# Performance work log

Hardware: AMD Instinct MI355X
Metric: run time of the kernel (lower is better)

Reference implementation:

```python
import jax, jax.numpy as jnp
import numpy as np

N, F_IN, F_OUT, K = 16384, 64, 64, 3


def setup_inputs() -> dict:
    key = jax.random.key(0)
    k1, k2, k3, k4 = jax.random.split(key, 4)
    x = jax.random.normal(k1, (N, F_IN), dtype=jnp.float32)
    # dense rescaled Laplacian; scale so repeated matmuls stay numerically tame
    L_tilde = jax.random.normal(k2, (N, N), dtype=jnp.float32) / np.float32(np.sqrt(N))
    stdv = 1.0 / np.sqrt(F_OUT)
    weights = jax.random.uniform(k3, (K + 1, F_IN, F_OUT), dtype=jnp.float32,
                                 minval=-stdv, maxval=stdv)
    bias = jax.random.uniform(k4, (F_OUT,), dtype=jnp.float32, minval=-stdv, maxval=stdv)
    return {"x": x, "L_tilde": L_tilde, "weights": weights, "bias": bias}


def reference(x, L_tilde, weights, bias):
    # Chebyshev recurrence: T0 = x, T1 = L@x, Tk = 2*L@T_{k-1} - T_{k-2}
    T_prev = x                                   # (N, F_in)
    out = T_prev @ weights[0]                    # (N, F_out)
    T_curr = L_tilde @ x
    out = out + T_curr @ weights[1]
    for k in range(2, K + 1):                    # fixed small K: python loop is fine
        T_next = 2.0 * (L_tilde @ T_curr) - T_prev
        out = out + T_next @ weights[k]
        T_prev, T_curr = T_curr, T_next
    return out + bias
```

## Files before the change

kernel.cpp:

```cpp
#include <hip/hip_runtime.h>
#include <cstddef>
#include <cstdint>

#define NN 16384
#define FF 64
#define BM 64
#define BK 64
#define SK 2
#define KHALF (NN / SK)
#define NC (KHALF / BK)

typedef __attribute__((ext_vector_type(8))) short bf16x8;
typedef __attribute__((ext_vector_type(4))) float f32x4;
typedef unsigned short ushort_t;

#define GLOBAL_AS __attribute__((address_space(1)))
#define LDS_AS    __attribute__((address_space(3)))

__device__ __forceinline__ void f32_split(float f, ushort_t& h, ushort_t& l) {
    unsigned u = __builtin_bit_cast(unsigned, f);
    h = (ushort_t)(u >> 16);
    float hf = __builtin_bit_cast(float, u & 0xFFFF0000u);
    float lo = f - hf;
    l = (ushort_t)(__builtin_bit_cast(unsigned, lo) >> 16);
}

__global__ __launch_bounds__(256) void convT(const float* __restrict__ T,
                                             ushort_t* __restrict__ Th,
                                             ushort_t* __restrict__ Tl)
{
    __shared__ float S[64][68];
    const int t = threadIdx.x;
    const int rb = blockIdx.x * 64;
    {
        const int row = t >> 2;
        const int c0 = (t & 3) * 16;
        const float* src = T + (size_t)(rb + row) * FF + c0;
        *(float4*)&S[row][c0 + 0]  = *(const float4*)(src + 0);
        *(float4*)&S[row][c0 + 4]  = *(const float4*)(src + 4);
        *(float4*)&S[row][c0 + 8]  = *(const float4*)(src + 8);
        *(float4*)&S[row][c0 + 12] = *(const float4*)(src + 12);
    }
    __syncthreads();
    const int cc = t >> 2;
    const int r0 = (t & 3) * 16;
    ushort_t hh[16], ll[16];
#pragma unroll
    for (int i = 0; i < 16; ++i)
        f32_split(S[r0 + i][cc], hh[i], ll[i]);
    unsigned wh[8], wl[8];
#pragma unroll
    for (int j = 0; j < 8; ++j) {
        wh[j] = (unsigned)hh[2 * j] | ((unsigned)hh[2 * j + 1] << 16);
        wl[j] = (unsigned)ll[2 * j] | ((unsigned)ll[2 * j + 1] << 16);
    }
    const size_t o = (size_t)cc * NN + rb + r0;
    *(uint4*)(Th + o)     = make_uint4(wh[0], wh[1], wh[2], wh[3]);
    *(uint4*)(Th + o + 8) = make_uint4(wh[4], wh[5], wh[6], wh[7]);
    *(uint4*)(Tl + o)     = make_uint4(wl[0], wl[1], wl[2], wl[3]);
    *(uint4*)(Tl + o + 8) = make_uint4(wl[4], wl[5], wl[6], wl[7]);
}

__global__ __launch_bounds__(256) void cheb_gemm_mfma(
    const float* __restrict__ L, const ushort_t* __restrict__ Th,
    const ushort_t* __restrict__ Tl, float* __restrict__ P)
{
    __shared__ ushort_t Ah[2][BM * BK];
    __shared__ ushort_t Al[2][BM * BK];
    __shared__ ushort_t Bh[2][FF * BK];
    __shared__ ushort_t Bl[2][FF * BK];

    const int tid  = threadIdx.x;
    const int lane = tid & 63;
    const int w    = tid >> 6;
    const int s    = blockIdx.x >> 8;
    const int m    = blockIdx.x & 255;
    const int row0g = m * BM;
    const int kbase = s * KHALF;

    const int wm = w >> 1, wn = w & 1;
    const int frow = lane & 15;
    const int fk8  = (lane >> 4) * 8;

    const int arow = w * 4 + (lane >> 4);
    const int akq  = lane & 15;
    const int axor = (arow & 7) << 4;

    const ushort_t* Tsrc = (w & 1) ? Tl : Th;
    const int boct0 = (w >> 1) * 4;

    f32x4 acc[2][2];
#pragma unroll
    for (int i = 0; i < 2; ++i)
#pragma unroll
        for (int j = 0; j < 2; ++j) acc[i][j] = (f32x4)0.f;

    float4 va[4];

    const float* Labase = L + (size_t)(row0g + arow) * NN + kbase + akq * 4;

#define ISSUE_B(c, slot)                                                        \
    {                                                                           \
        const size_t kc = (size_t)(c) * BK;                                     \
        char* bbase = (char*)((w & 1) ? Bl[slot] : Bh[slot]);                   \
        _Pragma("unroll")                                                       \
        for (int o = 0; o < 4; ++o) {                                           \
            const int oct = boct0 + o;                                          \
            const int col = oct * 8 + (lane >> 3);                              \
            const ushort_t* g = Tsrc + (size_t)col * NN + kbase + kc            \
                                + (((lane & 7) ^ (col & 7)) * 8);               \
            __builtin_amdgcn_global_load_lds((const GLOBAL_AS void*)g,          \
                (LDS_AS void*)(bbase + oct * 1024), 16, 0, 0);                  \
        }                                                                       \
    }

#define LOAD_A(c)                                                               \
    {                                                                           \
        const float* g = Labase + (size_t)(c) * BK;                             \
        va[0] = *(const float4*)(g);                                            \
        va[1] = *(const float4*)(g + (size_t)16 * NN);                          \
        va[2] = *(const float4*)(g + (size_t)32 * NN);                          \
        va[3] = *(const float4*)(g + (size_t)48 * NN);                          \
    }

#define CONV_WRITE_A(slot)                                                      \
    {                                                                           \
        char* ahb = (char*)Ah[slot];                                            \
        char* alb = (char*)Al[slot];                                            \
        _Pragma("unroll")                                                       \
        for (int p = 0; p < 4; ++p) {                                           \
            const int r = arow + p * 16;                                        \
            ushort_t h0, h1, h2, h3, l0, l1, l2, l3;                            \
            f32_split(va[p].x, h0, l0);                                         \
            f32_split(va[p].y, h1, l1);                                         \
            f32_split(va[p].z, h2, l2);                                         \
            f32_split(va[p].w, h3, l3);                                         \
            const unsigned hi01 = (unsigned)h0 | ((unsigned)h1 << 16);          \
            const unsigned hi23 = (unsigned)h2 | ((unsigned)h3 << 16);          \
            const unsigned lo01 = (unsigned)l0 | ((unsigned)l1 << 16);          \
            const unsigned lo23 = (unsigned)l2 | ((unsigned)l3 << 16);          \
            const int byte = (r * 128 + akq * 8) ^ axor;                        \
            *(uint2*)(ahb + byte) = make_uint2(hi01, hi23);                     \
            *(uint2*)(alb + byte) = make_uint2(lo01, lo23);                     \
        }                                                                       \
    }

    ISSUE_B(0, 0)
    LOAD_A(0)
    CONV_WRITE_A(0)
    __syncthreads();

    for (int c = 0; c < NC; ++c) {
        const int slot = c & 1;
        if (c + 1 < NC) {
            ISSUE_B(c + 1, slot ^ 1)
            LOAD_A(c + 1)
        }
        {
            const char* ahb = (const char*)Ah[slot];
            const char* alb = (const char*)Al[slot];
            const char* bhb = (const char*)Bh[slot];
            const char* blb = (const char*)Bl[slot];
#pragma unroll
            for (int ks = 0; ks < 2; ++ks) {
                const int kk = ks * 32 + fk8;
                bf16x8 Afh[2], Afl[2], Bfh[2], Bfl[2];
#pragma unroll
                for (int mt = 0; mt < 2; ++mt) {
                    const int row = wm * 32 + mt * 16 + frow;
                    const int off = (row * 128 + kk * 2) ^ ((row & 7) << 4);
                    Afh[mt] = *(const bf16x8*)(ahb + off);
                    Afl[mt] = *(const bf16x8*)(alb + off);
                }
#pragma unroll
                for (int nt = 0; nt < 2; ++nt) {
                    const int col = wn * 32 + nt * 16 + frow;
                    const int off = (col * 128 + kk * 2) ^ ((col & 7) << 4);
                    Bfh[nt] = *(const bf16x8*)(bhb + off);
                    Bfl[nt] = *(const bf16x8*)(blb + off);
                }
#pragma unroll
                for (int mt = 0; mt < 2; ++mt)
#pragma unroll
                    for (int nt = 0; nt < 2; ++nt) {
                        acc[mt][nt] = __builtin_amdgcn_mfma_f32_16x16x32_bf16(
                            Afh[mt], Bfh[nt], acc[mt][nt], 0, 0, 0);
                        acc[mt][nt] = __builtin_amdgcn_mfma_f32_16x16x32_bf16(
                            Afh[mt], Bfl[nt], acc[mt][nt], 0, 0, 0);
                        acc[mt][nt] = __builtin_amdgcn_mfma_f32_16x16x32_bf16(
                            Afl[mt], Bfh[nt], acc[mt][nt], 0, 0, 0);
                    }
            }
        }
        if (c + 1 < NC) CONV_WRITE_A(slot ^ 1)
        __syncthreads();
    }

    float* Pp = P + (size_t)s * NN * FF;
#pragma unroll
    for (int mt = 0; mt < 2; ++mt)
#pragma unroll
        for (int nt = 0; nt < 2; ++nt) {
            const int row = row0g + wm * 32 + mt * 16 + (lane >> 4) * 4;
            const int col = wn * 32 + nt * 16 + frow;
#pragma unroll
            for (int r = 0; r < 4; ++r)
                Pp[(size_t)(row + r) * FF + col] = acc[mt][nt][r];
        }
#undef ISSUE_B
#undef LOAD_A
#undef CONV_WRITE_A
}

__global__ __launch_bounds__(256) void reduce_axpby(
    const float* __restrict__ P0, const float* __restrict__ P1,
    const float* __restrict__ Tsub, float* __restrict__ Tout,
    float alpha, float beta)
{
    const int total = NN * FF / 4;
    for (int i = blockIdx.x * blockDim.x + threadIdx.x; i < total;
         i += gridDim.x * blockDim.x) {
        const float4 p0 = ((const float4*)P0)[i];
        const float4 p1 = ((const float4*)P1)[i];
        const float4 ts = ((const float4*)Tsub)[i];
        float4 o;
        o.x = alpha * (p0.x + p1.x) + beta * ts.x;
        o.y = alpha * (p0.y + p1.y) + beta * ts.y;
        o.z = alpha * (p0.z + p1.z) + beta * ts.z;
        o.w = alpha * (p0.w + p1.w) + beta * ts.w;
        ((float4*)Tout)[i] = o;
    }
}

__global__ __launch_bounds__(256) void out_update(
    const float* __restrict__ T, const float* __restrict__ Wk,
    const float* __restrict__ bias, float* __restrict__ out, int init)
{
    const int row = blockIdx.x * 4 + (threadIdx.x >> 6);
    const int col = threadIdx.x & 63;
    const float* t = T + (size_t)row * FF;
    const size_t oi = (size_t)row * FF + col;

    float acc = init ? bias[col] : out[oi];
#pragma unroll
    for (int f = 0; f < FF; ++f)
        acc += t[f] * Wk[f * FF + col];
    out[oi] = acc;
}

extern "C" void kernel_launch(void* const* d_in, const int* in_sizes, int n_in,
                              void* d_out, int out_size, void* d_ws, size_t ws_size,
                              hipStream_t stream)
{
    const float* x    = (const float*)d_in[0];
    const float* L    = (const float*)d_in[1];
    const float* W    = (const float*)d_in[2];
    const float* bias = (const float*)d_in[3];
    float* out = (float*)d_out;

    const size_t M1 = (size_t)NN * FF;
    float* wsf = (float*)d_ws;
    float* T1 = wsf;
    float* T2 = wsf + M1;
    float* T3 = wsf + 2 * M1;
    float* P0 = wsf + 3 * M1;
    float* P1 = wsf + 4 * M1;
    ushort_t* Tht = (ushort_t*)(wsf + 5 * M1);
    ushort_t* Tlt = Tht + M1;

    const dim3 gg(256 * SK), bg(256);
    const dim3 gc(NN / 64),  bc(256);
    const dim3 gr(512),      br(256);
    const dim3 go(NN / 4),   bo(256);

    out_update<<<go, bo, 0, stream>>>(x, W + 0 * FF * FF, bias, out, 1);

    convT<<<gc, bc, 0, stream>>>(x, Tht, Tlt);
    cheb_gemm_mfma<<<gg, bg, 0, stream>>>(L, Tht, Tlt, P0);
    reduce_axpby<<<gr, br, 0, stream>>>(P0, P1, x, T1, 1.f, 0.f);
    out_update<<<go, bo, 0, stream>>>(T1, W + 1 * FF * FF, bias, out, 0);

    convT<<<gc, bc, 0, stream>>>(T1, Tht, Tlt);
    cheb_gemm_mfma<<<gg, bg, 0, stream>>>(L, Tht, Tlt, P0);
    reduce_axpby<<<gr, br, 0, stream>>>(P0, P1, x, T2, 2.f, -1.f);
    out_update<<<go, bo, 0, stream>>>(T2, W + 2 * FF * FF, bias, out, 0);

    convT<<<gc, bc, 0, stream>>>(T2, Tht, Tlt);
    cheb_gemm_mfma<<<gg, bg, 0, stream>>>(L, Tht, Tlt, P0);
    reduce_axpby<<<gr, br, 0, stream>>>(P0, P1, T1, T3, 2.f, -1.f);
    out_update<<<go, bo, 0, stream>>>(T3, W + 3 * FF * FF, bias, out, 0);
}
```

Measured before the change: 747.5 us.

## Fuse reduce, output GEMM and bf16 split into one post-hop kernel; split-K 4

Replaces the separate reduce_axpby, out_update and convT launches after each Laplacian GEMM with a single post_hop kernel. Per 64-row tile it sums the split-K partials, applies the Chebyshev axpby, accumulates into the output through the weight matrix staged in LDS, and writes the transposed bf16 hi/lo operands for the next hop. The x@W0 term and the bias are folded into the first hop. Split-K goes from 2 to 4, giving the GEMM more blocks at the cost of more partial-sum traffic. Intermediates T2 and T3 are no longer stored, which cuts global memory round trips and launch count.

```diff
diff --git a/kernel.cpp b/kernel.cpp
--- a/kernel.cpp
+++ b/kernel.cpp
@@ -6,9 +6,9 @@
 #define FF 64
 #define BM 64
 #define BK 64
-#define SK 2
-#define KHALF (NN / SK)
-#define NC (KHALF / BK)
+#define SK 4
+#define KQ (NN / SK)
+#define NC (KQ / BK)
 
 typedef __attribute__((ext_vector_type(8))) short bf16x8;
 typedef __attribute__((ext_vector_type(4))) float f32x4;
@@ -76,7 +76,7 @@
     const int s    = blockIdx.x >> 8;
     const int m    = blockIdx.x & 255;
     const int row0g = m * BM;
-    const int kbase = s * KHALF;
+    const int kbase = s * KQ;
 
     const int wm = w >> 1, wn = w & 1;
     const int frow = lane & 15;
@@ -212,40 +212,162 @@
 #undef CONV_WRITE_A
 }
 
-__global__ __launch_bounds__(256) void reduce_axpby(
-    const float* __restrict__ P0, const float* __restrict__ P1,
-    const float* __restrict__ Tsub, float* __restrict__ Tout,
+__global__ __launch_bounds__(256) void post_hop(
+    const float* __restrict__ P,
+    const float* __restrict__ Tsub,
+    const float* __restrict__ Xin,
+    const float* __restrict__ W0w,
+    const float* __restrict__ Wkw,
+    const float* __restrict__ bias,
+    float* __restrict__ Tout,
+    ushort_t* __restrict__ Th, ushort_t* __restrict__ Tl,
+    float* __restrict__ out,
     float alpha, float beta)
 {
-    const int total = NN * FF / 4;
-    for (int i = blockIdx.x * blockDim.x + threadIdx.x; i < total;
-         i += gridDim.x * blockDim.x) {
-        const float4 p0 = ((const float4*)P0)[i];
-        const float4 p1 = ((const float4*)P1)[i];
-        const float4 ts = ((const float4*)Tsub)[i];
-        float4 o;
-        o.x = alpha * (p0.x + p1.x) + beta * ts.x;
-        o.y = alpha * (p0.y + p1.y) + beta * ts.y;
-        o.z = alpha * (p0.z + p1.z) + beta * ts.z;
-        o.w = alpha * (p0.w + p1.w) + beta * ts.w;
-        ((float4*)Tout)[i] = o;
-    }
-}
-
-__global__ __launch_bounds__(256) void out_update(
-    const float* __restrict__ T, const float* __restrict__ Wk,
-    const float* __restrict__ bias, float* __restrict__ out, int init)
-{
-    const int row = blockIdx.x * 4 + (threadIdx.x >> 6);
-    const int col = threadIdx.x & 63;
-    const float* t = T + (size_t)row * FF;
-    const size_t oi = (size_t)row * FF + col;
-
-    float acc = init ? bias[col] : out[oi];
-#pragma unroll
-    for (int f = 0; f < FF; ++f)
-        acc += t[f] * Wk[f * FF + col];
-    out[oi] = acc;
+    __shared__ float ST[64][68];
+    __shared__ float ST2[64][68];
+    __shared__ float WK[64][64];
+    __shared__ float WX[64][64];
+
+    const int tid = threadIdx.x;
+    const int rb = blockIdx.x * 64;
+    const size_t M1 = (size_t)NN * FF;
+
+    {
+        float4* wd = (float4*)&WK[0][0];
+        const float4* ws = (const float4*)Wkw;
+#pragma unroll
+        for (int j = 0; j < 4; ++j) wd[tid * 4 + j] = ws[tid * 4 + j];
+        if (Xin) {
+            float4* xd = (float4*)&WX[0][0];
+            const float4* xs = (const float4*)W0w;
+#pragma unroll
+            for (int j = 0; j < 4; ++j) xd[tid * 4 + j] = xs[tid * 4 + j];
+        }
+    }
+
+    {
+        const int arow = tid >> 2;
+        const int ac0 = (tid & 3) * 16;
+        const size_t rowOff = (size_t)(rb + arow) * FF + ac0;
+#pragma unroll
+        for (int j = 0; j < 4; ++j) {
+            const size_t o = rowOff + 4 * j;
+            float4 s  = *(const float4*)(P + o);
+            float4 p1 = *(const float4*)(P + M1 + o);
+            float4 p2 = *(const float4*)(P + 2 * M1 + o);
+            float4 p3 = *(const float4*)(P + 3 * M1 + o);
+            s.x += p1.x + p2.x + p3.x; s.y += p1.y + p2.y + p3.y;
+            s.z += p1.z + p2.z + p3.z; s.w += p1.w + p2.w + p3.w;
+            float4 t;
+            t.x = alpha * s.x; t.y = alpha * s.y;
+            t.z = alpha * s.z; t.w = alpha * s.w;
+            if (beta != 0.f) {
+                const float4 ts = *(const float4*)(Tsub + o);
+                t.x += beta * ts.x; t.y += beta * ts.y;
+                t.z += beta * ts.z; t.w += beta * ts.w;
+            }
+            if (Tout) *(float4*)(Tout + o) = t;
+            const int f0 = ac0 + 4 * j;
+            ST[f0 + 0][arow] = t.x; ST[f0 + 1][arow] = t.y;
+            ST[f0 + 2][arow] = t.z; ST[f0 + 3][arow] = t.w;
+            if (Xin) {
+                const float4 xv = *(const float4*)(Xin + o);
+                ST2[f0 + 0][arow] = xv.x; ST2[f0 + 1][arow] = xv.y;
+                ST2[f0 + 2][arow] = xv.z; ST2[f0 + 3][arow] = xv.w;
+            }
+        }
+    }
+    __syncthreads();
+
+    if (Th) {
+        const int cc = tid >> 2;
+        const int r0 = (tid & 3) * 16;
+        float vals[16];
+        *(float4*)&vals[0]  = *(const float4*)&ST[cc][r0];
+        *(float4*)&vals[4]  = *(const float4*)&ST[cc][r0 + 4];
+        *(float4*)&vals[8]  = *(const float4*)&ST[cc][r0 + 8];
+        *(float4*)&vals[12] = *(const float4*)&ST[cc][r0 + 12];
+        ushort_t hh[16], ll[16];
+#pragma unroll
+        for (int i = 0; i < 16; ++i) f32_split(vals[i], hh[i], ll[i]);
+        unsigned wh[8], wl[8];
+#pragma unroll
+        for (int j = 0; j < 8; ++j) {
+            wh[j] = (unsigned)hh[2 * j] | ((unsigned)hh[2 * j + 1] << 16);
+            wl[j] = (unsigned)ll[2 * j] | ((unsigned)ll[2 * j + 1] << 16);
+        }
+        const size_t o = (size_t)cc * NN + rb + r0;
+        *(uint4*)(Th + o)     = make_uint4(wh[0], wh[1], wh[2], wh[3]);
+        *(uint4*)(Th + o + 8) = make_uint4(wh[4], wh[5], wh[6], wh[7]);
+        *(uint4*)(Tl + o)     = make_uint4(wl[0], wl[1], wl[2], wl[3]);
+        *(uint4*)(Tl + o + 8) = make_uint4(wl[4], wl[5], wl[6], wl[7]);
+    }
+
+    {
+        const int tx = tid & 7;
+        const int ty = tid >> 3;
+        const int col0 = tx * 8;
+        const int row0 = ty * 2;
+        float acc[2][8];
+        if (Xin) {
+            const float4 b0 = *(const float4*)(bias + col0);
+            const float4 b1 = *(const float4*)(bias + col0 + 4);
+#pragma unroll
+            for (int r = 0; r < 2; ++r) {
+                acc[r][0] = b0.x; acc[r][1] = b0.y; acc[r][2] = b0.z; acc[r][3] = b0.w;
+                acc[r][4] = b1.x; acc[r][5] = b1.y; acc[r][6] = b1.z; acc[r][7] = b1.w;
+            }
+        } else {
+#pragma unroll
+            for (int r = 0; r < 2; ++r) {
+                const size_t o = (size_t)(rb + row0 + r) * FF + col0;
+                const float4 o0 = *(const float4*)(out + o);
+                const float4 o1 = *(const float4*)(out + o + 4);
+                acc[r][0] = o0.x; acc[r][1] = o0.y; acc[r][2] = o0.z; acc[r][3] = o0.w;
+                acc[r][4] = o1.x; acc[r][5] = o1.y; acc[r][6] = o1.z; acc[r][7] = o1.w;
+            }
+        }
+#pragma unroll
+        for (int f = 0; f < FF; ++f) {
+            const float2 lv = *(const float2*)&ST[f][row0];
+            const float4 w0 = *(const float4*)&WK[f][col0];
+            const float4 w1 = *(const float4*)&WK[f][col0 + 4];
+            acc[0][0] += lv.x * w0.x; acc[0][1] += lv.x * w0.y;
+            acc[0][2] += lv.x * w0.z; acc[0][3] += lv.x * w0.w;
+            acc[0][4] += lv.x * w1.x; acc[0][5] += lv.x * w1.y;
+            acc[0][6] += lv.x * w1.z; acc[0][7] += lv.x * w1.w;
+            acc[1][0] += lv.y * w0.x; acc[1][1] += lv.y * w0.y;
+            acc[1][2] += lv.y * w0.z; acc[1][3] += lv.y * w0.w;
+            acc[1][4] += lv.y * w1.x; acc[1][5] += lv.y * w1.y;
+            acc[1][6] += lv.y * w1.z; acc[1][7] += lv.y * w1.w;
+        }
+        if (Xin) {
+#pragma unroll
+            for (int f = 0; f < FF; ++f) {
+                const float2 lv = *(const float2*)&ST2[f][row0];
+                const float4 w0 = *(const float4*)&WX[f][col0];
+                const float4 w1 = *(const float4*)&WX[f][col0 + 4];
+                acc[0][0] += lv.x * w0.x; acc[0][1] += lv.x * w0.y;
+                acc[0][2] += lv.x * w0.z; acc[0][3] += lv.x * w0.w;
+                acc[0][4] += lv.x * w1.x; acc[0][5] += lv.x * w1.y;
+                acc[0][6] += lv.x * w1.z; acc[0][7] += lv.x * w1.w;
+                acc[1][0] += lv.y * w0.x; acc[1][1] += lv.y * w0.y;
+                acc[1][2] += lv.y * w0.z; acc[1][3] += lv.y * w0.w;
+                acc[1][4] += lv.y * w1.x; acc[1][5] += lv.y * w1.y;
+                acc[1][6] += lv.y * w1.z; acc[1][7] += lv.y * w1.w;
+            }
+        }
+#pragma unroll
+        for (int r = 0; r < 2; ++r) {
+            const size_t o = (size_t)(rb + row0 + r) * FF + col0;
+            float4 v0, v1;
+            v0.x = acc[r][0]; v0.y = acc[r][1]; v0.z = acc[r][2]; v0.w = acc[r][3];
+            v1.x = acc[r][4]; v1.y = acc[r][5]; v1.z = acc[r][6]; v1.w = acc[r][7];
+            *(float4*)(out + o) = v0;
+            *(float4*)(out + o + 4) = v1;
+        }
+    }
 }
 
 extern "C" void kernel_launch(void* const* d_in, const int* in_sizes, int n_in,
@@ -261,32 +383,21 @@
     const size_t M1 = (size_t)NN * FF;
     float* wsf = (float*)d_ws;
     float* T1 = wsf;
-    float* T2 = wsf + M1;
-    float* T3 = wsf + 2 * M1;
-    float* P0 = wsf + 3 * M1;
-    float* P1 = wsf + 4 * M1;
+    float* P  = wsf + M1;
     ushort_t* Tht = (ushort_t*)(wsf + 5 * M1);
     ushort_t* Tlt = Tht + M1;
 
     const dim3 gg(256 * SK), bg(256);
     const dim3 gc(NN / 64),  bc(256);
-    const dim3 gr(512),      br(256);
-    const dim3 go(NN / 4),   bo(256);
-
-    out_update<<<go, bo, 0, stream>>>(x, W + 0 * FF * FF, bias, out, 1);
 
     convT<<<gc, bc, 0, stream>>>(x, Tht, Tlt);
-    cheb_gemm_mfma<<<gg, bg, 0, stream>>>(L, Tht, Tlt, P0);
-    reduce_axpby<<<gr, br, 0, stream>>>(P0, P1, x, T1, 1.f, 0.f);
-    out_update<<<go, bo, 0, stream>>>(T1, W + 1 * FF * FF, bias, out, 0);
-
-    convT<<<gc, bc, 0, stream>>>(T1, Tht, Tlt);
-    cheb_gemm_mfma<<<gg, bg, 0, stream>>>(L, Tht, Tlt, P0);
-    reduce_axpby<<<gr, br, 0, stream>>>(P0, P1, x, T2, 2.f, -1.f);
-    out_update<<<go, bo, 0, stream>>>(T2, W + 2 * FF * FF, bias, out, 0);
-
-    convT<<<gc, bc, 0, stream>>>(T2, Tht, Tlt);
-    cheb_gemm_mfma<<<gg, bg, 0, stream>>>(L, Tht, Tlt, P0);
-    reduce_axpby<<<gr, br, 0, stream>>>(P0, P1, T1, T3, 2.f, -1.f);
-    out_update<<<go, bo, 0, stream>>>(T3, W + 3 * FF * FF, bias, out, 0);
+    cheb_gemm_mfma<<<gg, bg, 0, stream>>>(L, Tht, Tlt, P);
+    post_hop<<<gc, bc, 0, stream>>>(P, x, x, W + 0 * FF * FF, W + 1 * FF * FF,
+                                    bias, T1, Tht, Tlt, out, 1.f, 0.f);
+    cheb_gemm_mfma<<<gg, bg, 0, stream>>>(L, Tht, Tlt, P);
+    post_hop<<<gc, bc, 0, stream>>>(P, x, nullptr, nullptr, W + 2 * FF * FF,
+                                    bias, nullptr, Tht, Tlt, out, 2.f, -1.f);
+    cheb_gemm_mfma<<<gg, bg, 0, stream>>>(L, Tht, Tlt, P);
+    post_hop<<<gc, bc, 0, stream>>>(P, T1, nullptr, nullptr, W + 3 * FF * FF,
+                                    bias, nullptr, nullptr, nullptr, out, 2.f, -1.f);
 }
```

New measurement: 735.9 us. Within noise of the previous version (-1.5%).

## Drop split-K and fuse axpby, bf16 split and output projection into GEMM epilogue

Applied to the files above, without the earlier changes.

Removes the split-K partial buffers and the separate reduce, convert and out_update kernels. Each GEMM block now owns 32 full rows and does the rest in its epilogue: the Chebyshev axpby, writing the next hi/lo bf16 transposed operand, and accumulating T_k@W_k into the output. The x@W0 plus bias term is fused into the initial conversion kernel. This cuts launches and global round trips of intermediates. In exchange each block rereads the full T operand for only 32 rows, which doubles B-operand traffic from cache, and each wave does less MFMA work per loaded A tile.

```diff
diff --git a/kernel.cpp b/kernel.cpp
--- a/kernel.cpp
+++ b/kernel.cpp
@@ -4,11 +4,9 @@
 
 #define NN 16384
 #define FF 64
-#define BM 64
+#define BM 32
 #define BK 64
-#define SK 2
-#define KHALF (NN / SK)
-#define NC (KHALF / BK)
+#define NC (NN / BK)
 
 typedef __attribute__((ext_vector_type(8))) short bf16x8;
 typedef __attribute__((ext_vector_type(4))) float f32x4;
@@ -25,89 +23,128 @@
     l = (ushort_t)(__builtin_bit_cast(unsigned, lo) >> 16);
 }
 
-__global__ __launch_bounds__(256) void convT(const float* __restrict__ T,
-                                             ushort_t* __restrict__ Th,
-                                             ushort_t* __restrict__ Tl)
+__global__ __launch_bounds__(256) void convT_init(
+    const float* __restrict__ X, ushort_t* __restrict__ Th,
+    ushort_t* __restrict__ Tl, const float* __restrict__ W0,
+    const float* __restrict__ bias, float* __restrict__ out)
 {
     __shared__ float S[64][68];
+    __shared__ float W[64][64];
     const int t = threadIdx.x;
     const int rb = blockIdx.x * 64;
     {
         const int row = t >> 2;
         const int c0 = (t & 3) * 16;
-        const float* src = T + (size_t)(rb + row) * FF + c0;
+        const float* src = X + (size_t)(rb + row) * FF + c0;
         *(float4*)&S[row][c0 + 0]  = *(const float4*)(src + 0);
         *(float4*)&S[row][c0 + 4]  = *(const float4*)(src + 4);
         *(float4*)&S[row][c0 + 8]  = *(const float4*)(src + 8);
         *(float4*)&S[row][c0 + 12] = *(const float4*)(src + 12);
+        float4* wd = (float4*)&W[0][0];
+        const float4* ws = (const float4*)W0;
+#pragma unroll
+        for (int j = 0; j < 4; ++j) wd[t * 4 + j] = ws[t * 4 + j];
     }
     __syncthreads();
-    const int cc = t >> 2;
-    const int r0 = (t & 3) * 16;
-    ushort_t hh[16], ll[16];
-#pragma unroll
-    for (int i = 0; i < 16; ++i)
-        f32_split(S[r0 + i][cc], hh[i], ll[i]);
-    unsigned wh[8], wl[8];
-#pragma unroll
-    for (int j = 0; j < 8; ++j) {
-        wh[j] = (unsigned)hh[2 * j] | ((unsigned)hh[2 * j + 1] << 16);
-        wl[j] = (unsigned)ll[2 * j] | ((unsigned)ll[2 * j + 1] << 16);
-    }
-    const size_t o = (size_t)cc * NN + rb + r0;
-    *(uint4*)(Th + o)     = make_uint4(wh[0], wh[1], wh[2], wh[3]);
-    *(uint4*)(Th + o + 8) = make_uint4(wh[4], wh[5], wh[6], wh[7]);
-    *(uint4*)(Tl + o)     = make_uint4(wl[0], wl[1], wl[2], wl[3]);
-    *(uint4*)(Tl + o + 8) = make_uint4(wl[4], wl[5], wl[6], wl[7]);
+    {
+        const int cc = t >> 2;
+        const int r0 = (t & 3) * 16;
+        ushort_t hh[16], ll[16];
+#pragma unroll
+        for (int i = 0; i < 16; ++i) f32_split(S[r0 + i][cc], hh[i], ll[i]);
+        unsigned wh[8], wl[8];
+#pragma unroll
+        for (int j = 0; j < 8; ++j) {
+            wh[j] = (unsigned)hh[2 * j] | ((unsigned)hh[2 * j + 1] << 16);
+            wl[j] = (unsigned)ll[2 * j] | ((unsigned)ll[2 * j + 1] << 16);
+        }
+        const size_t o = (size_t)cc * NN + rb + r0;
+        *(uint4*)(Th + o)     = make_uint4(wh[0], wh[1], wh[2], wh[3]);
+        *(uint4*)(Th + o + 8) = make_uint4(wh[4], wh[5], wh[6], wh[7]);
+        *(uint4*)(Tl + o)     = make_uint4(wl[0], wl[1], wl[2], wl[3]);
+        *(uint4*)(Tl + o + 8) = make_uint4(wl[4], wl[5], wl[6], wl[7]);
+    }
+    {
+        const int row0 = (t >> 3) * 2;
+        const int col0 = (t & 7) * 8;
+        float acc[2][8];
+        const float4 b0 = *(const float4*)(bias + col0);
+        const float4 b1 = *(const float4*)(bias + col0 + 4);
+#pragma unroll
+        for (int r = 0; r < 2; ++r) {
+            acc[r][0] = b0.x; acc[r][1] = b0.y; acc[r][2] = b0.z; acc[r][3] = b0.w;
+            acc[r][4] = b1.x; acc[r][5] = b1.y; acc[r][6] = b1.z; acc[r][7] = b1.w;
+        }
+#pragma unroll
+        for (int f = 0; f < FF; ++f) {
+            const float x0 = S[row0][f];
+            const float x1 = S[row0 + 1][f];
+            const float4 w0 = *(const float4*)&W[f][col0];
+            const float4 w1 = *(const float4*)&W[f][col0 + 4];
+            acc[0][0] += x0 * w0.x; acc[0][1] += x0 * w0.y;
+            acc[0][2] += x0 * w0.z; acc[0][3] += x0 * w0.w;
+            acc[0][4] += x0 * w1.x; acc[0][5] += x0 * w1.y;
+            acc[0][6] += x0 * w1.z; acc[0][7] += x0 * w1.w;
+            acc[1][0] += x1 * w0.x; acc[1][1] += x1 * w0.y;
+            acc[1][2] += x1 * w0.z; acc[1][3] += x1 * w0.w;
+            acc[1][4] += x1 * w1.x; acc[1][5] += x1 * w1.y;
+            acc[1][6] += x1 * w1.z; acc[1][7] += x1 * w1.w;
+        }
+#pragma unroll
+        for (int r = 0; r < 2; ++r) {
+            const size_t o = (size_t)(rb + row0 + r) * FF + col0;
+            float4 v0, v1;
+            v0.x = acc[r][0]; v0.y = acc[r][1]; v0.z = acc[r][2]; v0.w = acc[r][3];
+            v1.x = acc[r][4]; v1.y = acc[r][5]; v1.z = acc[r][6]; v1.w = acc[r][7];
+            *(float4*)(out + o) = v0;
+            *(float4*)(out + o + 4) = v1;
+        }
+    }
 }
 
-__global__ __launch_bounds__(256) void cheb_gemm_mfma(
-    const float* __restrict__ L, const ushort_t* __restrict__ Th,
-    const ushort_t* __restrict__ Tl, float* __restrict__ P)
+__global__ __launch_bounds__(256) void cheb_hop(
+    const float* __restrict__ L,
+    const ushort_t* __restrict__ Th, const ushort_t* __restrict__ Tl,
+    ushort_t* __restrict__ Thn, ushort_t* __restrict__ Tln,
+    const float* __restrict__ Tsub, float* __restrict__ Tstore,
+    const float* __restrict__ Wk, float* __restrict__ out,
+    float alpha, float beta)
 {
-    __shared__ ushort_t Ah[2][BM * BK];
-    __shared__ ushort_t Al[2][BM * BK];
-    __shared__ ushort_t Bh[2][FF * BK];
-    __shared__ ushort_t Bl[2][FF * BK];
+    __shared__ char smem[49152];
+#define AHp(s) (smem + (s) * 4096)
+#define ALp(s) (smem + 8192 + (s) * 4096)
+#define BHp(s) (smem + 16384 + (s) * 8192)
+#define BLp(s) (smem + 32768 + (s) * 8192)
 
     const int tid  = threadIdx.x;
     const int lane = tid & 63;
     const int w    = tid >> 6;
-    const int s    = blockIdx.x >> 8;
-    const int m    = blockIdx.x & 255;
-    const int row0g = m * BM;
-    const int kbase = s * KHALF;
-
-    const int wm = w >> 1, wn = w & 1;
+    const int rb   = blockIdx.x * BM;
+
     const int frow = lane & 15;
     const int fk8  = (lane >> 4) * 8;
 
-    const int arow = w * 4 + (lane >> 4);
-    const int akq  = lane & 15;
-    const int axor = (arow & 7) << 4;
+    const int ar = tid >> 3;
+    const int akq = tid & 7;
 
     const ushort_t* Tsrc = (w & 1) ? Tl : Th;
     const int boct0 = (w >> 1) * 4;
 
-    f32x4 acc[2][2];
-#pragma unroll
-    for (int i = 0; i < 2; ++i)
-#pragma unroll
-        for (int j = 0; j < 2; ++j) acc[i][j] = (f32x4)0.f;
-
-    float4 va[4];
-
-    const float* Labase = L + (size_t)(row0g + arow) * NN + kbase + akq * 4;
+    f32x4 acc[2];
+    acc[0] = (f32x4)0.f; acc[1] = (f32x4)0.f;
+
+    float4 va0, va1;
+    const float* Labase = L + (size_t)(rb + ar) * NN + akq * 4;
 
 #define ISSUE_B(c, slot)                                                        \
     {                                                                           \
         const size_t kc = (size_t)(c) * BK;                                     \
-        char* bbase = (char*)((w & 1) ? Bl[slot] : Bh[slot]);                   \
+        char* bbase = (w & 1) ? BLp(slot) : BHp(slot);                          \
         _Pragma("unroll")                                                       \
         for (int o = 0; o < 4; ++o) {                                           \
             const int oct = boct0 + o;                                          \
             const int col = oct * 8 + (lane >> 3);                              \
-            const ushort_t* g = Tsrc + (size_t)col * NN + kbase + kc            \
+            const ushort_t* g = Tsrc + (size_t)col * NN + kc                    \
                                 + (((lane & 7) ^ (col & 7)) * 8);               \
             __builtin_amdgcn_global_load_lds((const GLOBAL_AS void*)g,          \
                 (LDS_AS void*)(bbase + oct * 1024), 16, 0, 0);                  \
@@ -117,32 +154,33 @@
 #define LOAD_A(c)                                                               \
     {                                                                           \
         const float* g = Labase + (size_t)(c) * BK;                             \
-        va[0] = *(const float4*)(g);                                            \
-        va[1] = *(const float4*)(g + (size_t)16 * NN);                          \
-        va[2] = *(const float4*)(g + (size_t)32 * NN);                          \
-        va[3] = *(const float4*)(g + (size_t)48 * NN);                          \
+        va0 = *(const float4*)(g);                                              \
+        va1 = *(const float4*)(g + 32);                                         \
     }
 
 #define CONV_WRITE_A(slot)                                                      \
     {                                                                           \
-        char* ahb = (char*)Ah[slot];                                            \
-        char* alb = (char*)Al[slot];                                            \
-        _Pragma("unroll")                                                       \
-        for (int p = 0; p < 4; ++p) {                                           \
-            const int r = arow + p * 16;                                        \
-            ushort_t h0, h1, h2, h3, l0, l1, l2, l3;                            \
-            f32_split(va[p].x, h0, l0);                                         \
-            f32_split(va[p].y, h1, l1);                                         \
-            f32_split(va[p].z, h2, l2);                                         \
-            f32_split(va[p].w, h3, l3);                                         \
-            const unsigned hi01 = (unsigned)h0 | ((unsigned)h1 << 16);          \
-            const unsigned hi23 = (unsigned)h2 | ((unsigned)h3 << 16);          \
-            const unsigned lo01 = (unsigned)l0 | ((unsigned)l1 << 16);          \
-            const unsigned lo23 = (unsigned)l2 | ((unsigned)l3 << 16);          \
-            const int byte = (r * 128 + akq * 8) ^ axor;                        \
-            *(uint2*)(ahb + byte) = make_uint2(hi01, hi23);                     \
-            *(uint2*)(alb + byte) = make_uint2(lo01, lo23);                     \
-        }                                                                       \
+        char* ahb = AHp(slot);                                                  \
+        char* alb = ALp(slot);                                                  \
+        ushort_t h0, h1, h2, h3, l0, l1, l2, l3;                                \
+        f32_split(va0.x, h0, l0); f32_split(va0.y, h1, l1);                     \
+        f32_split(va0.z, h2, l2); f32_split(va0.w, h3, l3);                     \
+        unsigned a01 = (unsigned)h0 | ((unsigned)h1 << 16);                     \
+        unsigned a23 = (unsigned)h2 | ((unsigned)h3 << 16);                     \
+        unsigned b01 = (unsigned)l0 | ((unsigned)l1 << 16);                     \
+        unsigned b23 = (unsigned)l2 | ((unsigned)l3 << 16);                     \
+        const int by0 = (ar * 128 + akq * 8) ^ ((ar & 7) << 4);                 \
+        *(uint2*)(ahb + by0) = make_uint2(a01, a23);                            \
+        *(uint2*)(alb + by0) = make_uint2(b01, b23);                            \
+        f32_split(va1.x, h0, l0); f32_split(va1.y, h1, l1);                     \
+        f32_split(va1.z, h2, l2); f32_split(va1.w, h3, l3);                     \
+        a01 = (unsigned)h0 | ((unsigned)h1 << 16);                              \
+        a23 = (unsigned)h2 | ((unsigned)h3 << 16);                              \
+        b01 = (unsigned)l0 | ((unsigned)l1 << 16);                              \
+        b23 = (unsigned)l2 | ((unsigned)l3 << 16);                              \
+        const int by1 = (ar * 128 + akq * 8 + 64) ^ ((ar & 7) << 4);            \
+        *(uint2*)(ahb + by1) = make_uint2(a01, a23);                            \
+        *(uint2*)(alb + by1) = make_uint2(b01, b23);                            \
     }
 
     ISSUE_B(0, 0)
@@ -157,95 +195,130 @@
             LOAD_A(c + 1)
         }
         {
-            const char* ahb = (const char*)Ah[slot];
-            const char* alb = (const char*)Al[slot];
-            const char* bhb = (const char*)Bh[slot];
-            const char* blb = (const char*)Bl[slot];
+            const char* ahb = AHp(slot);
+            const char* alb = ALp(slot);
+            const char* bhb = BHp(slot);
+            const char* blb = BLp(slot);
 #pragma unroll
             for (int ks = 0; ks < 2; ++ks) {
                 const int kk = ks * 32 + fk8;
-                bf16x8 Afh[2], Afl[2], Bfh[2], Bfl[2];
+                bf16x8 Afh[2], Afl[2], Bfh, Bfl;
 #pragma unroll
                 for (int mt = 0; mt < 2; ++mt) {
-                    const int row = wm * 32 + mt * 16 + frow;
+                    const int row = mt * 16 + frow;
                     const int off = (row * 128 + kk * 2) ^ ((row & 7) << 4);
                     Afh[mt] = *(const bf16x8*)(ahb + off);
                     Afl[mt] = *(const bf16x8*)(alb + off);
                 }
-#pragma unroll
-                for (int nt = 0; nt < 2; ++nt) {
-                    const int col = wn * 32 + nt * 16 + frow;
+                {
+                    const int col = w * 16 + frow;
                     const int off = (col * 128 + kk * 2) ^ ((col & 7) << 4);
-                    Bfh[nt] = *(const bf16x8*)(bhb + off);
-                    Bfl[nt] = *(const bf16x8*)(blb + off);
+                    Bfh = *(const bf16x8*)(bhb + off);
+                    Bfl = *(const bf16x8*)(blb + off);
                 }
 #pragma unroll
-                for (int mt = 0; mt < 2; ++mt)
-#pragma unroll
-                    for (int nt = 0; nt < 2; ++nt) {
-                        acc[mt][nt] = __builtin_amdgcn_mfma_f32_16x16x32_bf16(
-                            Afh[mt], Bfh[nt], acc[mt][nt], 0, 0, 0);
-                        acc[mt][nt] = __builtin_amdgcn_mfma_f32_16x16x32_bf16(
-                            Afh[mt], Bfl[nt], acc[mt][nt], 0, 0, 0);
-                        acc[mt][nt] = __builtin_amdgcn_mfma_f32_16x16x32_bf16(
-                            Afl[mt], Bfh[nt], acc[mt][nt], 0, 0, 0);
-                    }
+                for (int mt = 0; mt < 2; ++mt) {
+                    acc[mt] = __builtin_amdgcn_mfma_f32_16x16x32_bf16(
+                        Afh[mt], Bfh, acc[mt], 0, 0, 0);
+                    acc[mt] = __builtin_amdgcn_mfma_f32_16x16x32_bf16(
+                        Afh[mt], Bfl, acc[mt], 0, 0, 0);
+                    acc[mt] = __builtin_amdgcn_mfma_f32_16x16x32_bf16(
+                        Afl[mt], Bfh, acc[mt], 0, 0, 0);
+                }
             }
         }
         if (c + 1 < NC) CONV_WRITE_A(slot ^ 1)
         __syncthreads();
     }
 
-    float* Pp = P + (size_t)s * NN * FF;
-#pragma unroll
-    for (int mt = 0; mt < 2; ++mt)
-#pragma unroll
-        for (int nt = 0; nt < 2; ++nt) {
-            const int row = row0g + wm * 32 + mt * 16 + (lane >> 4) * 4;
-            const int col = wn * 32 + nt * 16 + frow;
+    float* ST  = (float*)(smem + 16384);
+    float* WKs = (float*)smem;
+
+    {
+        float4* wd = (float4*)WKs;
+        const float4* ws = (const float4*)Wk;
+#pragma unroll
+        for (int j = 0; j < 4; ++j) wd[tid * 4 + j] = ws[tid * 4 + j];
+
+        const int col = w * 16 + frow;
+        const int rowb = (lane >> 4) * 4;
+#pragma unroll
+        for (int mt = 0; mt < 2; ++mt)
 #pragma unroll
             for (int r = 0; r < 4; ++r)
-                Pp[(size_t)(row + r) * FF + col] = acc[mt][nt][r];
-        }
+                ST[col * 33 + mt * 16 + rowb + r] = acc[mt][r];
+    }
+    __syncthreads();
+
+    {
+        const int row = tid >> 3;
+        const int c0 = (tid & 7) * 8;
+        float tv[8];
+#pragma unroll
+        for (int j = 0; j < 8; ++j) tv[j] = alpha * ST[(c0 + j) * 33 + row];
+        if (beta != 0.f) {
+            const size_t o = (size_t)(rb + row) * FF + c0;
+            const float4 s0 = *(const float4*)(Tsub + o);
+            const float4 s1 = *(const float4*)(Tsub + o + 4);
+            tv[0] += beta * s0.x; tv[1] += beta * s0.y;
+            tv[2] += beta * s0.z; tv[3] += beta * s0.w;
+            tv[4] += beta * s1.x; tv[5] += beta * s1.y;
+            tv[6] += beta * s1.z; tv[7] += beta * s1.w;
+        }
+#pragma unroll
+        for (int j = 0; j < 8; ++j) ST[(c0 + j) * 33 + row] = tv[j];
+        if (Tstore) {
+            const size_t o = (size_t)(rb + row) * FF + c0;
+            float4 v0, v1;
+            v0.x = tv[0]; v0.y = tv[1]; v0.z = tv[2]; v0.w = tv[3];
+            v1.x = tv[4]; v1.y = tv[5]; v1.z = tv[6]; v1.w = tv[7];
+            *(float4*)(Tstore + o) = v0;
+            *(float4*)(Tstore + o + 4) = v1;
+        }
+    }
+    __syncthreads();
+
+    if (Thn) {
+        const int f = tid >> 2;
+        const int r0 = (tid & 3) * 8;
+        ushort_t hh[8], ll[8];
+#pragma unroll
+        for (int i = 0; i < 8; ++i) f32_split(ST[f * 33 + r0 + i], hh[i], ll[i]);
+        unsigned wh[4], wl[4];
+#pragma unroll
+        for (int j = 0; j < 4; ++j) {
+            wh[j] = (unsigned)hh[2 * j] | ((unsigned)hh[2 * j + 1] << 16);
+            wl[j] = (unsigned)ll[2 * j] | ((unsigned)ll[2 * j + 1] << 16);
+        }
+        const size_t o = (size_t)f * NN + rb + r0;
+        *(uint4*)(Thn + o) = make_uint4(wh[0], wh[1], wh[2], wh[3]);
+        *(uint4*)(Tln + o) = make_uint4(wl[0], wl[1], wl[2], wl[3]);
+    }
+
+    {
+        const int row = tid >> 3;
+        const int c0 = (tid & 7) * 8;
+        const size_t o = (size_t)(rb + row) * FF + c0;
+        float4 a0 = *(const float4*)(out + o);
+        float4 a1 = *(const float4*)(out + o + 4);
+#pragma unroll
+        for (int f = 0; f < FF; ++f) {
+            const float s = ST[f * 33 + row];
+            const float4 w0 = *(const float4*)&WKs[f * 64 + c0];
+            const float4 w1 = *(const float4*)&WKs[f * 64 + c0 + 4];
+            a0.x += s * w0.x; a0.y += s * w0.y; a0.z += s * w0.z; a0.w += s * w0.w;
+            a1.x += s * w1.x; a1.y += s * w1.y; a1.z += s * w1.z; a1.w += s * w1.w;
+        }
+        *(float4*)(out + o) = a0;
+        *(float4*)(out + o + 4) = a1;
+    }
 #undef ISSUE_B
 #undef LOAD_A
 #undef CONV_WRITE_A
-}
-
-__global__ __launch_bounds__(256) void reduce_axpby(
-    const float* __restrict__ P0, const float* __restrict__ P1,
-    const float* __restrict__ Tsub, float* __restrict__ Tout,
-    float alpha, float beta)
-{
-    const int total = NN * FF / 4;
-    for (int i = blockIdx.x * blockDim.x + threadIdx.x; i < total;
-         i += gridDim.x * blockDim.x) {
-        const float4 p0 = ((const float4*)P0)[i];
-        const float4 p1 = ((const float4*)P1)[i];
-        const float4 ts = ((const float4*)Tsub)[i];
-        float4 o;
-        o.x = alpha * (p0.x + p1.x) + beta * ts.x;
-        o.y = alpha * (p0.y + p1.y) + beta * ts.y;
-        o.z = alpha * (p0.z + p1.z) + beta * ts.z;
-        o.w = alpha * (p0.w + p1.w) + beta * ts.w;
-        ((float4*)Tout)[i] = o;
-    }
-}
-
-__global__ __launch_bounds__(256) void out_update(
-    const float* __restrict__ T, const float* __restrict__ Wk,
-    const float* __restrict__ bias, float* __restrict__ out, int init)
-{
-    const int row = blockIdx.x * 4 + (threadIdx.x >> 6);
-    const int col = threadIdx.x & 63;
-    const float* t = T + (size_t)row * FF;
-    const size_t oi = (size_t)row * FF + col;
-
-    float acc = init ? bias[col] : out[oi];
-#pragma unroll
-    for (int f = 0; f < FF; ++f)
-        acc += t[f] * Wk[f * FF + col];
-    out[oi] = acc;
+#undef AHp
+#undef ALp
+#undef BHp
+#undef BLp
 }
 
 extern "C" void kernel_launch(void* const* d_in, const int* in_sizes, int n_in,
@@ -261,32 +334,19 @@
     const size_t M1 = (size_t)NN * FF;
     float* wsf = (float*)d_ws;
     float* T1 = wsf;
-    float* T2 = wsf + M1;
-    float* T3 = wsf + 2 * M1;
-    float* P0 = wsf + 3 * M1;
-    float* P1 = wsf + 4 * M1;
-    ushort_t* Tht = (ushort_t*)(wsf + 5 * M1);
-    ushort_t* Tlt = Tht + M1;
-
-    const dim3 gg(256 * SK), bg(256);
-    const dim3 gc(NN / 64),  bc(256);
-    const dim3 gr(512),      br(256);
-    const dim3 go(NN / 4),   bo(256);
-
-    out_update<<<go, bo, 0, stream>>>(x, W + 0 * FF * FF, bias, out, 1);
-
-    convT<<<gc, bc, 0, stream>>>(x, Tht, Tlt);
-    cheb_gemm_mfma<<<gg, bg, 0, stream>>>(L, Tht, Tlt, P0);
-    reduce_axpby<<<gr, br, 0, stream>>>(P0, P1, x, T1, 1.f, 0.f);
-    out_update<<<go, bo, 0, stream>>>(T1, W + 1 * FF * FF, bias, out, 0);
-
-    convT<<<gc, bc, 0, stream>>>(T1, Tht, Tlt);
-    cheb_gemm_mfma<<<gg, bg, 0, stream>>>(L, Tht, Tlt, P0);
-    reduce_axpby<<<gr, br, 0, stream>>>(P0, P1, x, T2, 2.f, -1.f);
-    out_update<<<go, bo, 0, stream>>>(T2, W + 2 * FF * FF, bias, out, 0);
-
-    convT<<<gc, bc, 0, stream>>>(T2, Tht, Tlt);
-    cheb_gemm_mfma<<<gg, bg, 0, stream>>>(L, Tht, Tlt, P0);
-    reduce_axpby<<<gr, br, 0, stream>>>(P0, P1, T1, T3, 2.f, -1.f);
-    out_update<<<go, bo, 0, stream>>>(T3, W + 3 * FF * FF, bias, out, 0);
+    ushort_t* ThA = (ushort_t*)(wsf + M1);
+    ushort_t* TlA = ThA + M1;
+    ushort_t* ThB = TlA + M1;
+    ushort_t* TlB = ThB + M1;
+
+    const dim3 gc(NN / 64), bc(256);
+    const dim3 gg(NN / BM), bg(256);
+
+    convT_init<<<gc, bc, 0, stream>>>(x, ThA, TlA, W + 0 * FF * FF, bias, out);
+    cheb_hop<<<gg, bg, 0, stream>>>(L, ThA, TlA, ThB, TlB, x, T1,
+                                    W + 1 * FF * FF, out, 1.f, 0.f);
+    cheb_hop<<<gg, bg, 0, stream>>>(L, ThB, TlB, ThA, TlA, x, nullptr,
+                                    W + 2 * FF * FF, out, 2.f, -1.f);
+    cheb_hop<<<gg, bg, 0, stream>>>(L, ThA, TlA, nullptr, nullptr, T1, nullptr,
+                                    W + 3 * FF * FF, out, 2.f, -1.f);
 }
```

Result: slower. 938.9 us (+25.6%).

## Fuse reduction, output update and bf16 split into one post-hop kernel; split-K to 4

Applied to the files above, without the earlier changes.

Replaces the separate reduce, output-projection and transpose/bf16-split kernels with a single post_hop kernel per Chebyshev hop, and folds the initial output projection into the first conversion kernel. This removes intermediate T buffers and extra launches and global round-trips. Split-K is raised from 2 to 4 for the L GEMM, increasing the block count but also the partial-sum traffic that must be reduced.

```diff
diff --git a/kernel.cpp b/kernel.cpp
--- a/kernel.cpp
+++ b/kernel.cpp
@@ -6,9 +6,9 @@
 #define FF 64
 #define BM 64
 #define BK 64
-#define SK 2
-#define KHALF (NN / SK)
-#define NC (KHALF / BK)
+#define SK 4
+#define KQ (NN / SK)
+#define NC (KQ / BK)
 
 typedef __attribute__((ext_vector_type(8))) short bf16x8;
 typedef __attribute__((ext_vector_type(4))) float f32x4;
@@ -25,40 +25,83 @@
     l = (ushort_t)(__builtin_bit_cast(unsigned, lo) >> 16);
 }
 
-__global__ __launch_bounds__(256) void convT(const float* __restrict__ T,
-                                             ushort_t* __restrict__ Th,
-                                             ushort_t* __restrict__ Tl)
+__global__ __launch_bounds__(256) void convT_init(
+    const float* __restrict__ X, ushort_t* __restrict__ Th,
+    ushort_t* __restrict__ Tl, const float* __restrict__ W0,
+    const float* __restrict__ bias, float* __restrict__ out)
 {
     __shared__ float S[64][68];
+    __shared__ float W[64][64];
     const int t = threadIdx.x;
     const int rb = blockIdx.x * 64;
     {
         const int row = t >> 2;
         const int c0 = (t & 3) * 16;
-        const float* src = T + (size_t)(rb + row) * FF + c0;
+        const float* src = X + (size_t)(rb + row) * FF + c0;
         *(float4*)&S[row][c0 + 0]  = *(const float4*)(src + 0);
         *(float4*)&S[row][c0 + 4]  = *(const float4*)(src + 4);
         *(float4*)&S[row][c0 + 8]  = *(const float4*)(src + 8);
         *(float4*)&S[row][c0 + 12] = *(const float4*)(src + 12);
+        float4* wd = (float4*)&W[0][0];
+        const float4* ws = (const float4*)W0;
+#pragma unroll
+        for (int j = 0; j < 4; ++j) wd[t * 4 + j] = ws[t * 4 + j];
     }
     __syncthreads();
-    const int cc = t >> 2;
-    const int r0 = (t & 3) * 16;
-    ushort_t hh[16], ll[16];
-#pragma unroll
-    for (int i = 0; i < 16; ++i)
-        f32_split(S[r0 + i][cc], hh[i], ll[i]);
-    unsigned wh[8], wl[8];
-#pragma unroll
-    for (int j = 0; j < 8; ++j) {
-        wh[j] = (unsigned)hh[2 * j] | ((unsigned)hh[2 * j + 1] << 16);
-        wl[j] = (unsigned)ll[2 * j] | ((unsigned)ll[2 * j + 1] << 16);
-    }
-    const size_t o = (size_t)cc * NN + rb + r0;
-    *(uint4*)(Th + o)     = make_uint4(wh[0], wh[1], wh[2], wh[3]);
-    *(uint4*)(Th + o + 8) = make_uint4(wh[4], wh[5], wh[6], wh[7]);
-    *(uint4*)(Tl + o)     = make_uint4(wl[0], wl[1], wl[2], wl[3]);
-    *(uint4*)(Tl + o + 8) = make_uint4(wl[4], wl[5], wl[6], wl[7]);
+    {
+        const int cc = t >> 2;
+        const int r0 = (t & 3) * 16;
+        ushort_t hh[16], ll[16];
+#pragma unroll
+        for (int i = 0; i < 16; ++i) f32_split(S[r0 + i][cc], hh[i], ll[i]);
+        unsigned wh[8], wl[8];
+#pragma unroll
+        for (int j = 0; j < 8; ++j) {
+            wh[j] = (unsigned)hh[2 * j] | ((unsigned)hh[2 * j + 1] << 16);
+            wl[j] = (unsigned)ll[2 * j] | ((unsigned)ll[2 * j + 1] << 16);
+        }
+        const size_t o = (size_t)cc * NN + rb + r0;
+        *(uint4*)(Th + o)     = make_uint4(wh[0], wh[1], wh[2], wh[3]);
+        *(uint4*)(Th + o + 8) = make_uint4(wh[4], wh[5], wh[6], wh[7]);
+        *(uint4*)(Tl + o)     = make_uint4(wl[0], wl[1], wl[2], wl[3]);
+        *(uint4*)(Tl + o + 8) = make_uint4(wl[4], wl[5], wl[6], wl[7]);
+    }
+    {
+        const int row0 = (t >> 3) * 2;
+        const int col0 = (t & 7) * 8;
+        float acc[2][8];
+        const float4 b0 = *(const float4*)(bias + col0);
+        const float4 b1 = *(const float4*)(bias + col0 + 4);
+#pragma unroll
+        for (int r = 0; r < 2; ++r) {
+            acc[r][0] = b0.x; acc[r][1] = b0.y; acc[r][2] = b0.z; acc[r][3] = b0.w;
+            acc[r][4] = b1.x; acc[r][5] = b1.y; acc[r][6] = b1.z; acc[r][7] = b1.w;
+        }
+#pragma unroll
+        for (int f = 0; f < FF; ++f) {
+            const float x0 = S[row0][f];
+            const float x1 = S[row0 + 1][f];
+            const float4 w0 = *(const float4*)&W[f][col0];
+            const float4 w1 = *(const float4*)&W[f][col0 + 4];
+            acc[0][0] += x0 * w0.x; acc[0][1] += x0 * w0.y;
+            acc[0][2] += x0 * w0.z; acc[0][3] += x0 * w0.w;
+            acc[0][4] += x0 * w1.x; acc[0][5] += x0 * w1.y;
+            acc[0][6] += x0 * w1.z; acc[0][7] += x0 * w1.w;
+            acc[1][0] += x1 * w0.x; acc[1][1] += x1 * w0.y;
+            acc[1][2] += x1 * w0.z; acc[1][3] += x1 * w0.w;
+            acc[1][4] += x1 * w1.x; acc[1][5] += x1 * w1.y;
+            acc[1][6] += x1 * w1.z; acc[1][7] += x1 * w1.w;
+        }
+#pragma unroll
+        for (int r = 0; r < 2; ++r) {
+            const size_t o = (size_t)(rb + row0 + r) * FF + col0;
+            float4 v0, v1;
+            v0.x = acc[r][0]; v0.y = acc[r][1]; v0.z = acc[r][2]; v0.w = acc[r][3];
+            v1.x = acc[r][4]; v1.y = acc[r][5]; v1.z = acc[r][6]; v1.w = acc[r][7];
+            *(float4*)(out + o) = v0;
+            *(float4*)(out + o + 4) = v1;
+        }
+    }
 }
 
 __global__ __launch_bounds__(256) void cheb_gemm_mfma(
@@ -76,7 +119,7 @@
     const int s    = blockIdx.x >> 8;
     const int m    = blockIdx.x & 255;
     const int row0g = m * BM;
-    const int kbase = s * KHALF;
+    const int kbase = s * KQ;
 
     const int wm = w >> 1, wn = w & 1;
     const int frow = lane & 15;
@@ -212,40 +255,97 @@
 #undef CONV_WRITE_A
 }
 
-__global__ __launch_bounds__(256) void reduce_axpby(
-    const float* __restrict__ P0, const float* __restrict__ P1,
-    const float* __restrict__ Tsub, float* __restrict__ Tout,
+__global__ __launch_bounds__(256) void post_hop(
+    const float* __restrict__ P,
+    const float* __restrict__ Tsub, const float* __restrict__ Wk,
+    float* __restrict__ Tstore, ushort_t* __restrict__ Thn,
+    ushort_t* __restrict__ Tln, float* __restrict__ out,
     float alpha, float beta)
 {
-    const int total = NN * FF / 4;
-    for (int i = blockIdx.x * blockDim.x + threadIdx.x; i < total;
-         i += gridDim.x * blockDim.x) {
-        const float4 p0 = ((const float4*)P0)[i];
-        const float4 p1 = ((const float4*)P1)[i];
-        const float4 ts = ((const float4*)Tsub)[i];
-        float4 o;
-        o.x = alpha * (p0.x + p1.x) + beta * ts.x;
-        o.y = alpha * (p0.y + p1.y) + beta * ts.y;
-        o.z = alpha * (p0.z + p1.z) + beta * ts.z;
-        o.w = alpha * (p0.w + p1.w) + beta * ts.w;
-        ((float4*)Tout)[i] = o;
-    }
-}
-
-__global__ __launch_bounds__(256) void out_update(
-    const float* __restrict__ T, const float* __restrict__ Wk,
-    const float* __restrict__ bias, float* __restrict__ out, int init)
-{
-    const int row = blockIdx.x * 4 + (threadIdx.x >> 6);
-    const int col = threadIdx.x & 63;
-    const float* t = T + (size_t)row * FF;
-    const size_t oi = (size_t)row * FF + col;
-
-    float acc = init ? bias[col] : out[oi];
-#pragma unroll
-    for (int f = 0; f < FF; ++f)
-        acc += t[f] * Wk[f * FF + col];
-    out[oi] = acc;
+    __shared__ float ST[64][33];
+    __shared__ float WK[64][64];
+    const int t = threadIdx.x;
+    const int rb = blockIdx.x * 32;
+    const size_t M1 = (size_t)NN * FF;
+
+    {
+        float4* wd = (float4*)&WK[0][0];
+        const float4* ws = (const float4*)Wk;
+#pragma unroll
+        for (int j = 0; j < 4; ++j) wd[t * 4 + j] = ws[t * 4 + j];
+    }
+
+    const int row = t >> 3;
+    const int c0 = (t & 7) * 8;
+    const size_t o = (size_t)(rb + row) * FF + c0;
+
+    {
+        float tv[8];
+#pragma unroll
+        for (int half = 0; half < 2; ++half) {
+            const size_t oo = o + 4 * half;
+            float4 a0 = *(const float4*)(P + oo);
+            const float4 a1 = *(const float4*)(P + M1 + oo);
+            const float4 a2 = *(const float4*)(P + 2 * M1 + oo);
+            const float4 a3 = *(const float4*)(P + 3 * M1 + oo);
+            a0.x += a1.x + a2.x + a3.x; a0.y += a1.y + a2.y + a3.y;
+            a0.z += a1.z + a2.z + a3.z; a0.w += a1.w + a2.w + a3.w;
+            tv[4 * half + 0] = alpha * a0.x; tv[4 * half + 1] = alpha * a0.y;
+            tv[4 * half + 2] = alpha * a0.z; tv[4 * half + 3] = alpha * a0.w;
+        }
+        if (beta != 0.f) {
+            const float4 s0 = *(const float4*)(Tsub + o);
+            const float4 s1 = *(const float4*)(Tsub + o + 4);
+            tv[0] += beta * s0.x; tv[1] += beta * s0.y;
+            tv[2] += beta * s0.z; tv[3] += beta * s0.w;
+            tv[4] += beta * s1.x; tv[5] += beta * s1.y;
+            tv[6] += beta * s1.z; tv[7] += beta * s1.w;
+        }
+        if (Tstore) {
+            float4 v0, v1;
+            v0.x = tv[0]; v0.y = tv[1]; v0.z = tv[2]; v0.w = tv[3];
+            v1.x = tv[4]; v1.y = tv[5]; v1.z = tv[6]; v1.w = tv[7];
+            *(float4*)(Tstore + o) = v0;
+            *(float4*)(Tstore + o + 4) = v1;
+        }
+#pragma unroll
+        for (int j = 0; j < 8; ++j) ST[c0 + j][row] = tv[j];
+    }
+    __syncthreads();
+
+    if (Thn) {
+        const int f = t >> 2;
+        const int r0 = (t & 3) * 8;
+        ushort_t hh[8], ll[8];
+#pragma unroll
+        for (int i = 0; i < 8; ++i) f32_split(ST[f][r0 + i], hh[i], ll[i]);
+        unsigned wh[4], wl[4];
+#pragma unroll
+        for (int j = 0; j < 4; ++j) {
+            wh[j] = (unsigned)hh[2 * j] | ((unsigned)hh[2 * j + 1] << 16);
+            wl[j] = (unsigned)ll[2 * j] | ((unsigned)ll[2 * j + 1] << 16);
+        }
+        const size_t ob = (size_t)f * NN + rb + r0;
+        *(uint4*)(Thn + ob) = make_uint4(wh[0], wh[1], wh[2], wh[3]);
+        *(uint4*)(Tln + ob) = make_uint4(wl[0], wl[1], wl[2], wl[3]);
+    }
+
+    {
+        float4 a0 = *(const float4*)(out + o);
+        float4 a1 = *(const float4*)(out + o + 4);
+#pragma unroll
+        for (int f = 0; f < FF; ++f) {
+            const float sv = ST[f][row];
+            const float4 w0 = *(const float4*)&WK[f][c0];
+            const float4 w1 = *(const float4*)&WK[f][c0 + 4];
+            a0.x += sv * w0.x; a0.y += sv * w0.y;
+            a0.z += sv * w0.z; a0.w += sv * w0.w;
+            a1.x += sv * w1.x; a1.y += sv * w1.y;
+            a1.z += sv * w1.z; a1.w += sv * w1.w;
+        }
+        *(float4*)(out + o) = a0;
+        *(float4*)(out + o + 4) = a1;
+    }
 }
 
 extern "C" void kernel_launch(void* const* d_in, const int* in_sizes, int n_in,
@@ -261,32 +361,24 @@
     const size_t M1 = (size_t)NN * FF;
     float* wsf = (float*)d_ws;
     float* T1 = wsf;
-    float* T2 = wsf + M1;
-    float* T3 = wsf + 2 * M1;
-    float* P0 = wsf + 3 * M1;
-    float* P1 = wsf + 4 * M1;
-    ushort_t* Tht = (ushort_t*)(wsf + 5 * M1);
-    ushort_t* Tlt = Tht + M1;
-
-    const dim3 gg(256 * SK), bg(256);
-    const dim3 gc(NN / 64),  bc(256);
-    const dim3 gr(512),      br(256);
-    const dim3 go(NN / 4),   bo(256);
-
-    out_update<<<go, bo, 0, stream>>>(x, W + 0 * FF * FF, bias, out, 1);
-
-    convT<<<gc, bc, 0, stream>>>(x, Tht, Tlt);
-    cheb_gemm_mfma<<<gg, bg, 0, stream>>>(L, Tht, Tlt, P0);
-    reduce_axpby<<<gr, br, 0, stream>>>(P0, P1, x, T1, 1.f, 0.f);
-    out_update<<<go, bo, 0, stream>>>(T1, W + 1 * FF * FF, bias, out, 0);
-
-    convT<<<gc, bc, 0, stream>>>(T1, Tht, Tlt);
-    cheb_gemm_mfma<<<gg, bg, 0, stream>>>(L, Tht, Tlt, P0);
-    reduce_axpby<<<gr, br, 0, stream>>>(P0, P1, x, T2, 2.f, -1.f);
-    out_update<<<go, bo, 0, stream>>>(T2, W + 2 * FF * FF, bias, out, 0);
-
-    convT<<<gc, bc, 0, stream>>>(T2, Tht, Tlt);
-    cheb_gemm_mfma<<<gg, bg, 0, stream>>>(L, Tht, Tlt, P0);
-    reduce_axpby<<<gr, br, 0, stream>>>(P0, P1, T1, T3, 2.f, -1.f);
-    out_update<<<go, bo, 0, stream>>>(T3, W + 3 * FF * FF, bias, out, 0);
-}
+    float* P  = wsf + M1;
+    ushort_t* ThA = (ushort_t*)(wsf + 5 * M1);
+    ushort_t* TlA = ThA + M1;
+    ushort_t* ThB = TlA + M1;
+    ushort_t* TlB = ThB + M1;
+
+    const dim3 gc(NN / 64), bc(256);
+    const dim3 gg(SK * 256), bg(256);
+    const dim3 gp(NN / 32), bp(256);
+
+    convT_init<<<gc, bc, 0, stream>>>(x, ThA, TlA, W + 0 * FF * FF, bias, out);
+    cheb_gemm_mfma<<<gg, bg, 0, stream>>>(L, ThA, TlA, P);
+    post_hop<<<gp, bp, 0, stream>>>(P, x, W + 1 * FF * FF,
+                                    T1, ThB, TlB, out, 1.f, 0.f);
+    cheb_gemm_mfma<<<gg, bg, 0, stream>>>(L, ThB, TlB, P);
+    post_hop<<<gp, bp, 0, stream>>>(P, x, W + 2 * FF * FF,
+                                    nullptr, ThA, TlA, out, 2.f, -1.f);
+    cheb_gemm_mfma<<<gg, bg, 0, stream>>>(L, ThA, TlA, P);
+    post_hop<<<gp, bp, 0, stream>>>(P, T1, W + 3 * FF * FF,
+                                    nullptr, nullptr, nullptr, out, 2.f, -1.f);
+}
```

After: 725.9 us. 1.03x faster.
